# Optimization experiments

Measured on AMD Instinct MI355X. Metric: run time of the kernel, lower is better.

The kernel has to match this reference:

```python
import jax, jax.numpy as jnp
import numpy as np


def setup_inputs() -> dict:
    key = jax.random.key(0)
    k1, k2, k3, k4, k5 = jax.random.split(key, 5)
    N, M, K = 200000, 50, 4
    T = 1000.0
    ti = jnp.sort(jax.random.uniform(k1, (N,), dtype=jnp.float32) * T)
    mi = jax.random.randint(k2, (N,), 0, M, dtype=jnp.int64)
    mu_at_events = jax.random.uniform(k3, (N,), dtype=jnp.float32) * 0.5 + 0.05
    alpha = jax.random.uniform(k4, (K, M, M), dtype=jnp.float32) * 0.1
    gamma = jax.random.uniform(k5, (K,), dtype=jnp.float32) * 2.0 + 0.5
    return {"ti": ti, "mi": mi, "mu_at_events": mu_at_events, "alpha": alpha, "gamma": gamma}


def _hawkes_logsum(ti, mi, mu_at_events, alpha, gamma):
    # ti: [N] sorted event times; mi: [N] event types in [0, M)
    # alpha: [K, M, M]; gamma: [K]; mu_at_events: [N]
    N = ti.shape[0]
    M = alpha.shape[1]
    # inter-event gaps; dt[0] = 0 so the first event has zero excitation state
    dt = jnp.concatenate([jnp.zeros((1,), ti.dtype), ti[1:] - ti[:-1]])  # [N]
    a = jnp.exp(-gamma[None, :] * dt[:, None])  # [N, K] decay factors
    # one-hot of the PREVIOUS event's type (row 0 is all-zero, matching e_mi)
    prev_onehot = jnp.zeros((N, M), ti.dtype).at[jnp.arange(1, N), mi[:-1]].set(1.0)
    b = a[:, None, :] * prev_onehot[:, :, None]  # [N, M, K]

    # linear recurrence S_i = a_i * S_{i-1} + b_i via associative scan
    # combine((a1,b1),(a2,b2)) = (a1*a2, a2*b1 + b2)
    def combine(x, y):
        a1, b1 = x
        a2, b2 = y
        return (a1 * a2, a2[:, None, :] * b1 + b2)

    _, S = jax.lax.associative_scan(combine, (a, b))  # S: [N, M, K]
    # S[i, m, k] = sum_{j < i, m_j = m} exp(-gamma_k (t_i - t_j))
    alpha_at = alpha[:, mi, :]  # [K, N, M] rows of alpha for each event's type
    lam = mu_at_events + jnp.einsum('knm,nmk,k->n', alpha_at, S, gamma)  # [N]
    return jnp.sum(jnp.log(lam))


def reference(ti, mi, mu_at_events, alpha, gamma):
    return _hawkes_logsum(ti, mi, mu_at_events, alpha, gamma)
```

## Files before the change

kernel.cpp:

```cpp
#include <hip/hip_runtime.h>
#include <hip/hip_bf16.h>

#define CHUNK 256
#define MM 50
#define KK 4
#define STATE (MM*KK)
#define ASTRIDE 51
#define SUP 32
#define NSMAX 26
#define NSUB 8
#define SUBSZ 32

__device__ __forceinline__ unsigned short f2bf(float x) {
  unsigned u = __float_as_uint(x);
  u += 0x7fffu + ((u >> 16) & 1u);
  return (unsigned short)(u >> 16);
}

__global__ __launch_bounds__(256) void phase1(
    const float* __restrict__ ti, const int* __restrict__ mi,
    const float* __restrict__ gamma, float* __restrict__ chunkB,
    float* __restrict__ superB, float* __restrict__ out0, int N, int G) {
  int g = blockIdx.x, tid = threadIdx.x;
  if (g == 0 && tid == 0) out0[0] = 0.f;
  int l = g * CHUNK;
  int r = min(N, l + CHUNK);
  __shared__ float Bs[STATE];
  __shared__ float g4[KK];
  if (tid < STATE) Bs[tid] = 0.f;
  if (tid < KK) g4[tid] = gamma[tid];
  __syncthreads();
  float t_end = ti[r - 1];
  int j0 = (g == 0) ? 0 : (l - 1);
  int j = j0 + tid;
  if (j <= r - 2) {
    int m = mi[j];
    float dt = t_end - ti[j];
    #pragma unroll
    for (int k = 0; k < KK; ++k)
      atomicAdd(&Bs[m * KK + k], __expf(-g4[k] * dt));
  }
  __syncthreads();
  if (tid < STATE) {
    float v = Bs[tid];
    chunkB[(size_t)g * STATE + tid] = v;
    int sup = g / SUP;
    float gk = g4[tid & 3];
    float Tsup = ti[min(N, (sup + 1) * SUP * CHUNK) - 1];
    atomicAdd(&superB[(size_t)sup * STATE + tid], __expf(-gk * (Tsup - t_end)) * v);
  }
}

__global__ __launch_bounds__(256) void phase3(
    const float* __restrict__ ti, const int* __restrict__ mi,
    const float* __restrict__ mu, const float* __restrict__ alpha,
    const float* __restrict__ gamma, const float* __restrict__ chunkB,
    const float* __restrict__ superB, float* __restrict__ out, int N, int G) {
  int g = blockIdx.x, tid = threadIdx.x;
  int l = g * CHUNK;
  int r = min(N, l + CHUNK);
  int cnt = r - l;
  int sup = g / SUP;
  int g0 = sup * SUP;

  __shared__ unsigned P0[MM * ASTRIDE];
  __shared__ unsigned P1[MM * ASTRIDE];
  __shared__ __align__(16) float4 Fj[CHUNK];
  __shared__ int   cj[CHUNK];
  __shared__ __align__(16) float Q[NSUB][STATE];
  __shared__ float red[256];
  __shared__ float teL[SUP];
  __shared__ float tlast[NSMAX];

  float gk0 = gamma[0], gk1 = gamma[1], gk2 = gamma[2], gk3 = gamma[3];

  for (int i = tid; i < NSUB * STATE; i += 256) ((float*)Q)[i] = 0.f;

  for (int e = tid; e < MM * MM; e += 256) {
    int c = e / MM, cp = e - c * MM;
    float a0 = gk0 * alpha[e];
    float a1 = gk1 * alpha[2500 + e];
    float a2 = gk2 * alpha[5000 + e];
    float a3 = gk3 * alpha[7500 + e];
    P0[c * ASTRIDE + cp] = (unsigned)f2bf(a0) | ((unsigned)f2bf(a1) << 16);
    P1[c * ASTRIDE + cp] = (unsigned)f2bf(a2) | ((unsigned)f2bf(a3) << 16);
  }

  if (tid < SUP) {
    int c = g0 + tid;
    if (c < G) teL[tid] = ti[min(N, (c + 1) * CHUNK) - 1];
  } else if (tid >= 64 && tid < 64 + NSMAX) {
    int s = tid - 64;
    if (s < sup) tlast[s] = ti[min(N, (s + 1) * SUP * CHUNK) - 1];
  }

  int j = l - 1 + tid;
  float t_ref = ti[(g == 0) ? 0 : (l - 1)];
  float4 myF = make_float4(0.f, 0.f, 0.f, 0.f);
  int myc = 0;
  bool valid = (j >= 0) && (j <= r - 2);
  if (valid) {
    myc = mi[j];
    float tj = ti[j] - t_ref;
    myF = make_float4(__expf(gk0 * tj), __expf(gk1 * tj),
                      __expf(gk2 * tj), __expf(gk3 * tj));
  }
  cj[tid] = myc;
  Fj[tid] = myF;
  __syncthreads();

  if (valid) {
    float* q = &Q[tid >> 5][myc * KK];
    atomicAdd(q + 0, myF.x); atomicAdd(q + 1, myF.y);
    atomicAdd(q + 2, myF.z); atomicAdd(q + 3, myF.w);
  }

  float S = 0.f;
  if (tid < STATE) {
    float gk = gamma[tid & 3];
    int nloc = g - g0;
    #pragma unroll 4
    for (int u = 0; u < nloc; ++u)
      S += __expf(-gk * (t_ref - teL[u])) * chunkB[(size_t)(g0 + u) * STATE + tid];
    #pragma unroll 4
    for (int s = 0; s < sup; ++s)
      S += __expf(-gk * (t_ref - tlast[s])) * superB[(size_t)s * STATE + tid];
  }
  __syncthreads();

  if (tid < STATE) {
    float run = S;
    #pragma unroll
    for (int q = 0; q < NSUB; ++q) {
      float t = Q[q][tid];
      Q[q][tid] = run;
      run += t;
    }
  }
  __syncthreads();

  float local = 0.f;
  if (tid < cnt) {
    int n = l + tid;
    int c_n = mi[n];
    int rowb = c_n * ASTRIDE;
    const float4* wb = (const float4*)&Q[tid >> 5][0];
    float4 acc = make_float4(0.f, 0.f, 0.f, 0.f);
    #pragma unroll 5
    for (int m = 0; m < MM; ++m) {
      unsigned p0 = P0[rowb + m];
      unsigned p1 = P1[rowb + m];
      float4 w = wb[m];
      acc.x += __uint_as_float(p0 << 16)         * w.x;
      acc.y += __uint_as_float(p0 & 0xffff0000u) * w.y;
      acc.z += __uint_as_float(p1 << 16)         * w.z;
      acc.w += __uint_as_float(p1 & 0xffff0000u) * w.w;
    }
    #pragma unroll 4
    for (int s = (tid & ~(SUBSZ - 1)); s <= tid; ++s) {
      unsigned p0 = P0[rowb + cj[s]];
      unsigned p1 = P1[rowb + cj[s]];
      float4 f = Fj[s];
      acc.x += __uint_as_float(p0 << 16)         * f.x;
      acc.y += __uint_as_float(p0 & 0xffff0000u) * f.y;
      acc.z += __uint_as_float(p1 << 16)         * f.z;
      acc.w += __uint_as_float(p1 & 0xffff0000u) * f.w;
    }
    float tn = ti[n] - t_ref;
    float lam = mu[n]
              + __expf(-gk0 * tn) * acc.x + __expf(-gk1 * tn) * acc.y
              + __expf(-gk2 * tn) * acc.z + __expf(-gk3 * tn) * acc.w;
    local = __logf(lam);
  }
  red[tid] = local;
  __syncthreads();
  for (int off = 128; off > 0; off >>= 1) {
    if (tid < off) red[tid] += red[tid + off];
    __syncthreads();
  }
  if (tid == 0) atomicAdd(out, red[0]);
}

extern "C" void kernel_launch(void* const* d_in, const int* in_sizes, int n_in,
                              void* d_out, int out_size, void* d_ws, size_t ws_size,
                              hipStream_t stream) {
  const float* ti    = (const float*)d_in[0];
  const int*   mi    = (const int*)d_in[1];
  const float* mu    = (const float*)d_in[2];
  const float* alpha = (const float*)d_in[3];
  const float* gamma = (const float*)d_in[4];
  float* out = (float*)d_out;
  int N = in_sizes[0];
  int G = (N + CHUNK - 1) / CHUNK;
  int nS = (G + SUP - 1) / SUP;
  float* chunkB = (float*)d_ws;
  float* superB = chunkB + (size_t)G * STATE;

  hipMemsetAsync(superB, 0, (size_t)nS * STATE * sizeof(float), stream);
  phase1<<<G, 256, 0, stream>>>(ti, mi, gamma, chunkB, superB, out, N, G);
  phase3<<<G, 256, 0, stream>>>(ti, mi, mu, alpha, gamma, chunkB, superB, out, N, G);
}
```

Measured before the change: 95.42 us.

## Merge two-phase Hawkes kernel into one launch with inter-block flag synchronization

Folds the chunk-summary phase into the main kernel: each block computes its chunk's end-state from the shared Q accumulators it already builds, publishes it with release flags and per-superchunk counters, then spin-waits on its predecessors before the prefix and intensity computation. The final log-sum is accumulated in workspace and written by the last block to finish. This removes a kernel launch and the duplicated reads and exp work of the old phase1. In exchange it depends on all 782 blocks being co-resident or scheduled in order to avoid deadlock, and it adds spin-wait latency.

Result: slower. 184.8 us (+93.7%).

```diff
diff --git a/kernel.cpp b/kernel.cpp
--- a/kernel.cpp
+++ b/kernel.cpp
@@ -8,6 +8,7 @@
 #define ASTRIDE 51
 #define SUP 32
 #define NSMAX 26
+#define GMAX 832
 #define NSUB 8
 #define SUBSZ 32
 
@@ -17,51 +18,24 @@
   return (unsigned short)(u >> 16);
 }
 
-__global__ __launch_bounds__(256) void phase1(
-    const float* __restrict__ ti, const int* __restrict__ mi,
-    const float* __restrict__ gamma, float* __restrict__ chunkB,
-    float* __restrict__ superB, float* __restrict__ out0, int N, int G) {
-  int g = blockIdx.x, tid = threadIdx.x;
-  if (g == 0 && tid == 0) out0[0] = 0.f;
-  int l = g * CHUNK;
-  int r = min(N, l + CHUNK);
-  __shared__ float Bs[STATE];
-  __shared__ float g4[KK];
-  if (tid < STATE) Bs[tid] = 0.f;
-  if (tid < KK) g4[tid] = gamma[tid];
-  __syncthreads();
-  float t_end = ti[r - 1];
-  int j0 = (g == 0) ? 0 : (l - 1);
-  int j = j0 + tid;
-  if (j <= r - 2) {
-    int m = mi[j];
-    float dt = t_end - ti[j];
-    #pragma unroll
-    for (int k = 0; k < KK; ++k)
-      atomicAdd(&Bs[m * KK + k], __expf(-g4[k] * dt));
-  }
-  __syncthreads();
-  if (tid < STATE) {
-    float v = Bs[tid];
-    chunkB[(size_t)g * STATE + tid] = v;
-    int sup = g / SUP;
-    float gk = g4[tid & 3];
-    float Tsup = ti[min(N, (sup + 1) * SUP * CHUNK) - 1];
-    atomicAdd(&superB[(size_t)sup * STATE + tid], __expf(-gk * (Tsup - t_end)) * v);
-  }
-}
-
-__global__ __launch_bounds__(256) void phase3(
+__device__ __forceinline__ float agload(const float* p) {
+  return __hip_atomic_load(p, __ATOMIC_RELAXED, __HIP_MEMORY_SCOPE_AGENT);
+}
+
+__global__ __launch_bounds__(256, 4) void hawkes_merged(
     const float* __restrict__ ti, const int* __restrict__ mi,
     const float* __restrict__ mu, const float* __restrict__ alpha,
-    const float* __restrict__ gamma, const float* __restrict__ chunkB,
-    const float* __restrict__ superB, float* __restrict__ out, int N, int G) {
+    const float* __restrict__ gamma,
+    float* __restrict__ superB, int* __restrict__ cflag, int* __restrict__ supcnt,
+    float* __restrict__ wsSum, int* __restrict__ done, float* __restrict__ chunkB,
+    float* __restrict__ out, int N, int G) {
   int g = blockIdx.x, tid = threadIdx.x;
   int l = g * CHUNK;
   int r = min(N, l + CHUNK);
   int cnt = r - l;
   int sup = g / SUP;
   int g0 = sup * SUP;
+  int nloc = g - g0;
 
   __shared__ unsigned P0[MM * ASTRIDE];
   __shared__ unsigned P1[MM * ASTRIDE];
@@ -114,21 +88,51 @@
     atomicAdd(q + 0, myF.x); atomicAdd(q + 1, myF.y);
     atomicAdd(q + 2, myF.z); atomicAdd(q + 3, myF.w);
   }
-
-  float S = 0.f;
+  __syncthreads();
+
   if (tid < STATE) {
-    float gk = gamma[tid & 3];
-    int nloc = g - g0;
+    int kk = tid & 3;
+    float gk = (kk == 0) ? gk0 : (kk == 1) ? gk1 : (kk == 2) ? gk2 : gk3;
+    float t_end = ti[r - 1];
+    float Dend = __expf(-gk * (t_end - t_ref));
+    float b = 0.f;
+    #pragma unroll
+    for (int q = 0; q < NSUB; ++q) b += Q[q][tid];
+    float v = Dend * b;
+    __hip_atomic_store(&chunkB[(size_t)g * STATE + tid], v,
+                       __ATOMIC_RELAXED, __HIP_MEMORY_SCOPE_AGENT);
+    float Tsup = ti[min(N, (sup + 1) * SUP * CHUNK) - 1];
+    atomicAdd(&superB[(size_t)sup * STATE + tid], __expf(-gk * (Tsup - t_end)) * v);
+  }
+  __syncthreads();
+  if (tid == 0) {
+    __hip_atomic_store(&cflag[g], 1, __ATOMIC_RELEASE, __HIP_MEMORY_SCOPE_AGENT);
+    __hip_atomic_fetch_add(&supcnt[sup], 1, __ATOMIC_RELEASE, __HIP_MEMORY_SCOPE_AGENT);
+  }
+
+  if (tid < nloc) {
+    while (__hip_atomic_load(&cflag[g0 + tid], __ATOMIC_ACQUIRE,
+                             __HIP_MEMORY_SCOPE_AGENT) == 0)
+      __builtin_amdgcn_s_sleep(2);
+  }
+  if (tid >= 64 && tid < 64 + sup) {
+    int s = tid - 64;
+    while (__hip_atomic_load(&supcnt[s], __ATOMIC_ACQUIRE,
+                             __HIP_MEMORY_SCOPE_AGENT) < SUP)
+      __builtin_amdgcn_s_sleep(2);
+  }
+  __syncthreads();
+
+  if (tid < STATE) {
+    int kk = tid & 3;
+    float gk = (kk == 0) ? gk0 : (kk == 1) ? gk1 : (kk == 2) ? gk2 : gk3;
+    float S = 0.f;
     #pragma unroll 4
     for (int u = 0; u < nloc; ++u)
-      S += __expf(-gk * (t_ref - teL[u])) * chunkB[(size_t)(g0 + u) * STATE + tid];
+      S += __expf(-gk * (t_ref - teL[u])) * agload(&chunkB[(size_t)(g0 + u) * STATE + tid]);
     #pragma unroll 4
     for (int s = 0; s < sup; ++s)
-      S += __expf(-gk * (t_ref - tlast[s])) * superB[(size_t)s * STATE + tid];
-  }
-  __syncthreads();
-
-  if (tid < STATE) {
+      S += __expf(-gk * (t_ref - tlast[s])) * agload(&superB[(size_t)s * STATE + tid]);
     float run = S;
     #pragma unroll
     for (int q = 0; q < NSUB; ++q) {
@@ -178,7 +182,11 @@
     if (tid < off) red[tid] += red[tid + off];
     __syncthreads();
   }
-  if (tid == 0) atomicAdd(out, red[0]);
+  if (tid == 0) {
+    atomicAdd(wsSum, red[0]);
+    int old = __hip_atomic_fetch_add(done, 1, __ATOMIC_ACQ_REL, __HIP_MEMORY_SCOPE_AGENT);
+    if (old == G - 1) out[0] = agload(wsSum);
+  }
 }
 
 extern "C" void kernel_launch(void* const* d_in, const int* in_sizes, int n_in,
@@ -192,11 +200,17 @@
   float* out = (float*)d_out;
   int N = in_sizes[0];
   int G = (N + CHUNK - 1) / CHUNK;
-  int nS = (G + SUP - 1) / SUP;
-  float* chunkB = (float*)d_ws;
-  float* superB = chunkB + (size_t)G * STATE;
-
-  hipMemsetAsync(superB, 0, (size_t)nS * STATE * sizeof(float), stream);
-  phase1<<<G, 256, 0, stream>>>(ti, mi, gamma, chunkB, superB, out, N, G);
-  phase3<<<G, 256, 0, stream>>>(ti, mi, mu, alpha, gamma, chunkB, superB, out, N, G);
-}
+
+  float* superB = (float*)d_ws;
+  int*   cflag  = (int*)(superB + (size_t)NSMAX * STATE);
+  int*   supcnt = cflag + GMAX;
+  float* wsSum  = (float*)(supcnt + NSMAX);
+  int*   done   = (int*)(wsSum + 1);
+  size_t zbytes = (size_t)((char*)(done + 1) - (char*)d_ws);
+  float* chunkB = (float*)((char*)d_ws + ((zbytes + 15) & ~15ull));
+
+  hipMemsetAsync(d_ws, 0, zbytes, stream);
+  hawkes_merged<<<G, 256, 0, stream>>>(ti, mi, mu, alpha, gamma,
+                                       superB, cflag, supcnt, wsSum, done, chunkB,
+                                       out, N, G);
+}
```
